# Optimization experiments

Measured on AMD Instinct MI355X. Metric: run time of the kernel, lower is better.

The kernel has to match this reference:

```python
import jax, jax.numpy as jnp
import numpy as np

K = 9          # census/SAD window (block_size arg of photometric_loss)
R = K // 2
EPS = 0.5      # loss_eps


def _grid_sample_disp(pattern, disp):
    """Disparity warp: pattern_proj[b,0,v,u] = bilinear(pattern, x=u-disp, y=v).
    Matches F.grid_sample(padding_mode='border', align_corners=True) since
    uv1 = 2*(x/(W-1)-0.5) maps back to pixel coord x exactly, and y is the row index.
    pattern: [1,1,H,W], disp: [B,H,W] -> [B,1,H,W]."""
    H, W = pattern.shape[-2:]
    B = disp.shape[0]
    u0 = jnp.arange(W, dtype=disp.dtype)
    x = u0[None, None, :] - disp                 # source x coordinate, [B,H,W]
    x = jnp.clip(x, 0.0, W - 1.0)                # border padding
    x0 = jnp.floor(x)
    w = x - x0                                   # bilinear weight
    i0 = x0.astype(jnp.int32)
    i1 = jnp.minimum(i0 + 1, W - 1)
    p = jnp.broadcast_to(pattern[0, 0], (B, H, W))
    g0 = jnp.take_along_axis(p, i0, axis=2)
    g1 = jnp.take_along_axis(p, i1, axis=2)
    return ((1.0 - w) * g0 + w * g1)[:, None]    # [B,1,H,W]


def _census_sad(a, b, eps):
    """Per-pixel census-SAD over a KxK window.
    Soft census: c(n, center) = (n-center)/(eps+|n-center|); per pixel the loss is
    mean over window offsets of |c_a - c_b|, out-of-bounds offsets skipped.
    a, b: [B,1,H,W] -> [B,1,H,W]."""
    B, C, H, W = a.shape
    pa = jnp.pad(a, ((0, 0), (0, 0), (R, R), (R, R)))
    pb = jnp.pad(b, ((0, 0), (0, 0), (R, R), (R, R)))
    vm = jnp.pad(jnp.ones((H, W), a.dtype), ((R, R), (R, R)))  # validity mask
    acc = jnp.zeros_like(a)
    for dh in range(-R, R + 1):
        for dw in range(-R, R + 1):
            na = pa[:, :, R + dh:R + dh + H, R + dw:R + dw + W]
            nb = pb[:, :, R + dh:R + dh + H, R + dw:R + dw + W]
            da = na - a
            db = nb - b
            ca = da / (eps + jnp.abs(da))
            cb = db / (eps + jnp.abs(db))
            v = vm[R + dh:R + dh + H, R + dw:R + dw + W]
            acc = acc + v * jnp.abs(ca - cb)
    return acc / (K * K)


def reference(disp0, im, pattern):
    B = disp0.shape[0]
    H, W = im.shape[-2:]
    d = disp0.reshape(B, H, W)
    pattern_proj = _grid_sample_disp(pattern, d)
    diff = _census_sad(pattern_proj, im, EPS)
    mask = jnp.ones_like(im)                     # std is None
    val = (mask * diff).sum() / mask.sum()
    return val, pattern_proj


def setup_inputs():
    key = jax.random.key(0)
    k1, k2, k3 = jax.random.split(key, 3)
    B, H, W = 32, 512, 640
    disp0 = jax.random.uniform(k1, (B, 1, H, W), dtype=jnp.float32) * 64.0
    im = jax.random.uniform(k2, (B, 1, H, W), dtype=jnp.float32)
    pattern = jax.random.uniform(k3, (1, 1, H, W), dtype=jnp.float32)
    return {"disp0": disp0, "im": im, "pattern": pattern}
```

## Files before the change

kernel.cpp:

```cpp
#include <hip/hip_runtime.h>

#define Wd 640
#define Hd 512
#define NB 32
#define TW 64
#define TH 16
#define RR 4
#define SW 72
constexpr int TILES_X = Wd / TW;
constexpr int TILES_Y = Hd / TH;
constexpr int PLANE  = (TH + RR) * SW;
constexpr float EPSC = 0.5f;

__global__ __launch_bounds__(256)
void warp_kernel(const float* __restrict__ disp, const float* __restrict__ pattern,
                 float* __restrict__ proj)
{
    int gid = blockIdx.x * 256 + threadIdx.x;
    int n = gid * 4;
    float4 d4 = *(const float4*)(disp + n);
    int u = n % Wd;
    int rowbase = ((n / Wd) % Hd) * Wd;
    float dv[4] = {d4.x, d4.y, d4.z, d4.w};
    #pragma unroll
    for (int j = 0; j < 4; ++j) {
        float x = (float)(u + j) - dv[j];
        x = fminf(fmaxf(x, 0.f), (float)(Wd - 1));
        float x0 = floorf(x);
        float w = x - x0;
        int i0 = (int)x0;
        int i1 = min(i0 + 1, Wd - 1);
        float g0 = pattern[rowbase + i0];
        float g1 = pattern[rowbase + i1];
        proj[n + j] = fmaf(w, g1 - g0, g0);
    }
}

__device__ __forceinline__ void census_ne(float na, float nb, float ac, float bc,
                                          float& n, float& e)
{
    float da = na - ac;
    float db = nb - bc;
    float d1 = EPSC + fabsf(da);
    float d2 = EPSC + fabsf(db);
    n = fmaf(da, d2, -(db * d1));
    e = d1 * d2;
}

__device__ __forceinline__ float comb4(float n1, float e1, float n2, float e2,
                                       float n3, float e3, float n4, float e4)
{
    float e12 = e1 * e2, e34 = e3 * e4;
    float s12 = fmaf(fabsf(n2), e1, fabsf(n1) * e2);
    float s34 = fmaf(fabsf(n4), e3, fabsf(n3) * e4);
    float t   = fmaf(s34, e12, s12 * e34);
    return t * __builtin_amdgcn_rcpf(e12 * e34);
}

#define WLOAD(DH) \
    a0=p0[(DH)*SW+0]; a1=p0[(DH)*SW+1]; a2=p0[(DH)*SW+2]; a3=p0[(DH)*SW+3]; \
    a4=p0[(DH)*SW+4]; a5=p0[(DH)*SW+5]; a6=p0[(DH)*SW+6]; a7=p0[(DH)*SW+7]; \
    a8=p0[(DH)*SW+8]; \
    b0=p1[(DH)*SW+0]; b1=p1[(DH)*SW+1]; b2=p1[(DH)*SW+2]; b3=p1[(DH)*SW+3]; \
    b4=p1[(DH)*SW+4]; b5=p1[(DH)*SW+5]; b6=p1[(DH)*SW+6]; b7=p1[(DH)*SW+7]; \
    b8=p1[(DH)*SW+8];

#define CENTERRT(P) { \
    cA##P = a4; cB##P = b4; \
    float n0,e0,n1,e1,n2,e2,n3,e3; \
    census_ne(a5,b5,a4,b4,n0,e0); \
    census_ne(a6,b6,a4,b4,n1,e1); \
    census_ne(a7,b7,a4,b4,n2,e2); \
    census_ne(a8,b8,a4,b4,n3,e3); \
    if constexpr (EC) { n0*=mm[5]; n1*=mm[6]; n2*=mm[7]; n3*=mm[8]; } \
    acc##P += comb4(n0,e0,n1,e1,n2,e2,n3,e3); }

#define ROWP(P) { \
    float n0,e0,n1,e1,n2,e2,n3,e3,n4,e4,n5,e5,n6,e6,n7,e7,n8,e8; \
    census_ne(a0,b0,cA##P,cB##P,n0,e0); \
    census_ne(a1,b1,cA##P,cB##P,n1,e1); \
    census_ne(a2,b2,cA##P,cB##P,n2,e2); \
    census_ne(a3,b3,cA##P,cB##P,n3,e3); \
    census_ne(a4,b4,cA##P,cB##P,n4,e4); \
    census_ne(a5,b5,cA##P,cB##P,n5,e5); \
    census_ne(a6,b6,cA##P,cB##P,n6,e6); \
    census_ne(a7,b7,cA##P,cB##P,n7,e7); \
    census_ne(a8,b8,cA##P,cB##P,n8,e8); \
    if constexpr (EC) { n0*=mm[0]; n1*=mm[1]; n2*=mm[2]; n3*=mm[3]; \
                        n5*=mm[5]; n6*=mm[6]; n7*=mm[7]; n8*=mm[8]; } \
    acc##P += comb4(n0,e0,n1,e1,n2,e2,n3,e3); \
    acc##P += comb4(n5,e5,n6,e6,n7,e7,n8,e8); \
    acc##P += fabsf(n4) * __builtin_amdgcn_rcpf(e4); }

template<bool EC>
__device__ __forceinline__ float strip_sum(const float* p0, const float* p1,
                                           int gr0, int x)
{
    float mm[9];
    if constexpr (EC) {
        #pragma unroll
        for (int i = 0; i < 9; ++i)
            mm[i] = ((unsigned)(x + i - 4) < (unsigned)Wd) ? 1.f : 0.f;
    }
    float a0,a1,a2,a3,a4,a5,a6,a7,a8, b0,b1,b2,b3,b4,b5,b6,b7,b8;
    float cA0,cA1,cA2,cA3, cB0,cB1,cB2,cB3;
    float acc0=0.f, acc1=0.f, acc2=0.f, acc3=0.f;

    WLOAD(0) CENTERRT(0)
    WLOAD(1) CENTERRT(1) ROWP(0)
    WLOAD(2) CENTERRT(2) ROWP(0) ROWP(1)
    WLOAD(3) CENTERRT(3) ROWP(0) ROWP(1) ROWP(2)
    if (gr0 + 4 < Hd) { WLOAD(4) ROWP(0) ROWP(1) ROWP(2) ROWP(3) }
    if (gr0 + 5 < Hd) { WLOAD(5) ROWP(1) ROWP(2) ROWP(3) }
    if (gr0 + 6 < Hd) { WLOAD(6) ROWP(2) ROWP(3) }
    if (gr0 + 7 < Hd) { WLOAD(7) ROWP(3) }
    return (acc0 + acc1) + (acc2 + acc3);
}

__global__ __launch_bounds__(256)
void census_kernel(const float* __restrict__ proj, const float* __restrict__ im,
                   float* __restrict__ partial)
{
    __shared__ float lds[2 * PLANE];

    const int tU = blockIdx.x, tV = blockIdx.y, b = blockIdx.z;
    const int tid = threadIdx.x;
    const float* pb = proj + (size_t)b * (Hd * Wd);
    const float* ib = im   + (size_t)b * (Hd * Wd);
    const int v0  = tV * TH;
    const int u0g = tU * TW - RR;

    const bool edgeC = (tU == 0) | (tU == TILES_X - 1);
    const bool edgeR = (tV == TILES_Y - 1);

    if (!edgeC && !edgeR) {
        const float* pbase = pb + v0 * Wd + u0g;
        const float* ibase = ib + v0 * Wd + u0g;
        for (int f = tid; f < (TH + RR) * 18; f += 256) {
            int r = f / 18;
            int c = (f - 18 * r) * 4;
            *(float4*)&lds[r * SW + c]         = *(const float4*)(pbase + r * Wd + c);
            *(float4*)&lds[PLANE + r * SW + c] = *(const float4*)(ibase + r * Wd + c);
        }
    } else {
        for (int idx = tid; idx < PLANE; idx += 256) {
            int r = idx / SW;
            int c = idx - r * SW;
            int gv = min(v0 + r, Hd - 1);
            int gu = min(max(u0g + c, 0), Wd - 1);
            int off = gv * Wd + gu;
            lds[idx]         = pb[off];
            lds[PLANE + idx] = ib[off];
        }
    }
    __syncthreads();

    const int lane = tid & 63;
    const int w    = tid >> 6;
    const int x    = tU * TW + lane;
    const int gr0  = v0 + 4 * w;
    const float* p0 = lds + (4 * w) * SW + lane;
    const float* p1 = p0 + PLANE;

    float acc = edgeC ? strip_sum<true >(p0, p1, gr0, x)
                      : strip_sum<false>(p0, p1, gr0, x);

    #pragma unroll
    for (int o = 32; o; o >>= 1) acc += __shfl_down(acc, o);
    __shared__ float wsum[4];
    if (lane == 0) wsum[w] = acc;
    __syncthreads();
    if (tid == 0) {
        float s = wsum[0] + wsum[1] + wsum[2] + wsum[3];
        partial[((int)blockIdx.z * gridDim.y + blockIdx.y) * gridDim.x + blockIdx.x] = s;
    }
}

__global__ __launch_bounds__(1024)
void final_reduce(const float* __restrict__ partial, float* __restrict__ out)
{
    const int n = NB * TILES_Y * TILES_X;
    double s = 0.0;
    for (int i = threadIdx.x; i < n; i += 1024) s += (double)partial[i];
    __shared__ double sm[1024];
    sm[threadIdx.x] = s;
    __syncthreads();
    for (int st = 512; st; st >>= 1) {
        if (threadIdx.x < st) sm[threadIdx.x] += sm[threadIdx.x + st];
        __syncthreads();
    }
    if (threadIdx.x == 0) {
        out[0] = (float)(sm[0] * (2.0 / (81.0 * (double)NB * Hd * Wd)));
    }
}

extern "C" void kernel_launch(void* const* d_in, const int* in_sizes, int n_in,
                              void* d_out, int out_size, void* d_ws, size_t ws_size,
                              hipStream_t stream)
{
    const float* disp    = (const float*)d_in[0];
    const float* im      = (const float*)d_in[1];
    const float* pattern = (const float*)d_in[2];
    float* out  = (float*)d_out;
    float* proj = out + 1;
    float* partial = (float*)d_ws;

    const int npx = NB * Hd * Wd;
    warp_kernel<<<npx / (256 * 4), 256, 0, stream>>>(disp, pattern, proj);

    dim3 grid(TILES_X, TILES_Y, NB);
    census_kernel<<<grid, 256, 0, stream>>>(proj, im, partial);

    final_reduce<<<1, 1024, 0, stream>>>(partial, out);
}
```

Baseline: 143.1 us.

## Fuse disparity warp into census kernel and switch to 4-pixel-per-thread tiling

Removes the separate warp kernel and computes the bilinear-warped pattern tile, halo included, directly into shared memory inside the census kernel. Interior pixels are also written to the proj output. This avoids writing proj and then reading it back from global memory. The tile height grows to 32 rows and each thread now handles 4 horizontal pixels with float4 LDS reads, without the previous row-reuse scheme. Halo pixels are warped redundantly across tiles, and the proj stores are scalar and misaligned (proj = out+1).

```diff
diff --git a/kernel.cpp b/kernel.cpp
--- a/kernel.cpp
+++ b/kernel.cpp
@@ -4,37 +4,14 @@
 #define Hd 512
 #define NB 32
 #define TW 64
-#define TH 16
+#define TH2 32
 #define RR 4
 #define SW 72
+#define ROWS (TH2 + RR)
 constexpr int TILES_X = Wd / TW;
-constexpr int TILES_Y = Hd / TH;
-constexpr int PLANE  = (TH + RR) * SW;
+constexpr int TILES_Y = Hd / TH2;
+constexpr int NBLK = TILES_X * TILES_Y * NB;
 constexpr float EPSC = 0.5f;
-
-__global__ __launch_bounds__(256)
-void warp_kernel(const float* __restrict__ disp, const float* __restrict__ pattern,
-                 float* __restrict__ proj)
-{
-    int gid = blockIdx.x * 256 + threadIdx.x;
-    int n = gid * 4;
-    float4 d4 = *(const float4*)(disp + n);
-    int u = n % Wd;
-    int rowbase = ((n / Wd) % Hd) * Wd;
-    float dv[4] = {d4.x, d4.y, d4.z, d4.w};
-    #pragma unroll
-    for (int j = 0; j < 4; ++j) {
-        float x = (float)(u + j) - dv[j];
-        x = fminf(fmaxf(x, 0.f), (float)(Wd - 1));
-        float x0 = floorf(x);
-        float w = x - x0;
-        int i0 = (int)x0;
-        int i1 = min(i0 + 1, Wd - 1);
-        float g0 = pattern[rowbase + i0];
-        float g1 = pattern[rowbase + i1];
-        proj[n + j] = fmaf(w, g1 - g0, g0);
-    }
-}
 
 __device__ __forceinline__ void census_ne(float na, float nb, float ac, float bc,
                                           float& n, float& e)
@@ -57,118 +34,175 @@
     return t * __builtin_amdgcn_rcpf(e12 * e34);
 }
 
-#define WLOAD(DH) \
-    a0=p0[(DH)*SW+0]; a1=p0[(DH)*SW+1]; a2=p0[(DH)*SW+2]; a3=p0[(DH)*SW+3]; \
-    a4=p0[(DH)*SW+4]; a5=p0[(DH)*SW+5]; a6=p0[(DH)*SW+6]; a7=p0[(DH)*SW+7]; \
-    a8=p0[(DH)*SW+8]; \
-    b0=p1[(DH)*SW+0]; b1=p1[(DH)*SW+1]; b2=p1[(DH)*SW+2]; b3=p1[(DH)*SW+3]; \
-    b4=p1[(DH)*SW+4]; b5=p1[(DH)*SW+5]; b6=p1[(DH)*SW+6]; b7=p1[(DH)*SW+7]; \
-    b8=p1[(DH)*SW+8];
-
-#define CENTERRT(P) { \
-    cA##P = a4; cB##P = b4; \
+#define PX_ROW(J, ACC) { \
+    float n0,e0,n1,e1,n2,e2,n3,e3,n4,e4,n5,e5,n6,e6,n7,e7,n8,e8; \
+    census_ne(wa[(J)+0],wb[(J)+0],ca[J],cb[J],n0,e0); \
+    census_ne(wa[(J)+1],wb[(J)+1],ca[J],cb[J],n1,e1); \
+    census_ne(wa[(J)+2],wb[(J)+2],ca[J],cb[J],n2,e2); \
+    census_ne(wa[(J)+3],wb[(J)+3],ca[J],cb[J],n3,e3); \
+    census_ne(wa[(J)+4],wb[(J)+4],ca[J],cb[J],n4,e4); \
+    census_ne(wa[(J)+5],wb[(J)+5],ca[J],cb[J],n5,e5); \
+    census_ne(wa[(J)+6],wb[(J)+6],ca[J],cb[J],n6,e6); \
+    census_ne(wa[(J)+7],wb[(J)+7],ca[J],cb[J],n7,e7); \
+    census_ne(wa[(J)+8],wb[(J)+8],ca[J],cb[J],n8,e8); \
+    if constexpr (EC) { n0*=m[(J)+0]; n1*=m[(J)+1]; n2*=m[(J)+2]; n3*=m[(J)+3]; \
+                        n5*=m[(J)+5]; n6*=m[(J)+6]; n7*=m[(J)+7]; n8*=m[(J)+8]; } \
+    if constexpr (ER) { n0*=mv; n1*=mv; n2*=mv; n3*=mv; n4*=mv; \
+                        n5*=mv; n6*=mv; n7*=mv; n8*=mv; } \
+    ACC += comb4(n0,e0,n1,e1,n2,e2,n3,e3); \
+    ACC += comb4(n5,e5,n6,e6,n7,e7,n8,e8); \
+    ACC = fmaf(fabsf(n4), __builtin_amdgcn_rcpf(e4), ACC); }
+
+#define PX_CTR(J, ACC) { \
     float n0,e0,n1,e1,n2,e2,n3,e3; \
-    census_ne(a5,b5,a4,b4,n0,e0); \
-    census_ne(a6,b6,a4,b4,n1,e1); \
-    census_ne(a7,b7,a4,b4,n2,e2); \
-    census_ne(a8,b8,a4,b4,n3,e3); \
-    if constexpr (EC) { n0*=mm[5]; n1*=mm[6]; n2*=mm[7]; n3*=mm[8]; } \
-    acc##P += comb4(n0,e0,n1,e1,n2,e2,n3,e3); }
-
-#define ROWP(P) { \
-    float n0,e0,n1,e1,n2,e2,n3,e3,n4,e4,n5,e5,n6,e6,n7,e7,n8,e8; \
-    census_ne(a0,b0,cA##P,cB##P,n0,e0); \
-    census_ne(a1,b1,cA##P,cB##P,n1,e1); \
-    census_ne(a2,b2,cA##P,cB##P,n2,e2); \
-    census_ne(a3,b3,cA##P,cB##P,n3,e3); \
-    census_ne(a4,b4,cA##P,cB##P,n4,e4); \
-    census_ne(a5,b5,cA##P,cB##P,n5,e5); \
-    census_ne(a6,b6,cA##P,cB##P,n6,e6); \
-    census_ne(a7,b7,cA##P,cB##P,n7,e7); \
-    census_ne(a8,b8,cA##P,cB##P,n8,e8); \
-    if constexpr (EC) { n0*=mm[0]; n1*=mm[1]; n2*=mm[2]; n3*=mm[3]; \
-                        n5*=mm[5]; n6*=mm[6]; n7*=mm[7]; n8*=mm[8]; } \
-    acc##P += comb4(n0,e0,n1,e1,n2,e2,n3,e3); \
-    acc##P += comb4(n5,e5,n6,e6,n7,e7,n8,e8); \
-    acc##P += fabsf(n4) * __builtin_amdgcn_rcpf(e4); }
-
-template<bool EC>
-__device__ __forceinline__ float strip_sum(const float* p0, const float* p1,
-                                           int gr0, int x)
-{
-    float mm[9];
+    census_ne(wa[(J)+5],wb[(J)+5],ca[J],cb[J],n0,e0); \
+    census_ne(wa[(J)+6],wb[(J)+6],ca[J],cb[J],n1,e1); \
+    census_ne(wa[(J)+7],wb[(J)+7],ca[J],cb[J],n2,e2); \
+    census_ne(wa[(J)+8],wb[(J)+8],ca[J],cb[J],n3,e3); \
+    if constexpr (EC) { n0*=m[(J)+5]; n1*=m[(J)+6]; n2*=m[(J)+7]; n3*=m[(J)+8]; } \
+    ACC += comb4(n0,e0,n1,e1,n2,e2,n3,e3); }
+
+template<bool EC, bool ER>
+__device__ __forceinline__ float strip_sum(const float (*sa)[SW], const float (*sb)[SW],
+                                           int ty, int tx, int ub, int v0)
+{
+    float m[12];
     if constexpr (EC) {
         #pragma unroll
-        for (int i = 0; i < 9; ++i)
-            mm[i] = ((unsigned)(x + i - 4) < (unsigned)Wd) ? 1.f : 0.f;
-    }
-    float a0,a1,a2,a3,a4,a5,a6,a7,a8, b0,b1,b2,b3,b4,b5,b6,b7,b8;
-    float cA0,cA1,cA2,cA3, cB0,cB1,cB2,cB3;
-    float acc0=0.f, acc1=0.f, acc2=0.f, acc3=0.f;
-
-    WLOAD(0) CENTERRT(0)
-    WLOAD(1) CENTERRT(1) ROWP(0)
-    WLOAD(2) CENTERRT(2) ROWP(0) ROWP(1)
-    WLOAD(3) CENTERRT(3) ROWP(0) ROWP(1) ROWP(2)
-    if (gr0 + 4 < Hd) { WLOAD(4) ROWP(0) ROWP(1) ROWP(2) ROWP(3) }
-    if (gr0 + 5 < Hd) { WLOAD(5) ROWP(1) ROWP(2) ROWP(3) }
-    if (gr0 + 6 < Hd) { WLOAD(6) ROWP(2) ROWP(3) }
-    if (gr0 + 7 < Hd) { WLOAD(7) ROWP(3) }
+        for (int i = 0; i < 12; ++i)
+            m[i] = ((unsigned)(ub + i - 4) < (unsigned)Wd) ? 1.f : 0.f;
+    }
+    const int cu = 4 * tx;
+    float acc0 = 0.f, acc1 = 0.f, acc2 = 0.f, acc3 = 0.f;
+
+    for (int rb = ty; rb < TH2; rb += 16) {
+        float ca[4], cb[4], wa[12], wb[12];
+        {
+            float4 A1 = *(const float4*)&sa[rb][cu + 4];
+            float4 A2 = *(const float4*)&sa[rb][cu + 8];
+            float4 B1 = *(const float4*)&sb[rb][cu + 4];
+            float4 B2 = *(const float4*)&sb[rb][cu + 8];
+            wa[4]=A1.x; wa[5]=A1.y; wa[6]=A1.z; wa[7]=A1.w;
+            wa[8]=A2.x; wa[9]=A2.y; wa[10]=A2.z; wa[11]=A2.w;
+            wb[4]=B1.x; wb[5]=B1.y; wb[6]=B1.z; wb[7]=B1.w;
+            wb[8]=B2.x; wb[9]=B2.y; wb[10]=B2.z; wb[11]=B2.w;
+            ca[0]=wa[4]; ca[1]=wa[5]; ca[2]=wa[6]; ca[3]=wa[7];
+            cb[0]=wb[4]; cb[1]=wb[5]; cb[2]=wb[6]; cb[3]=wb[7];
+            PX_CTR(0, acc0) PX_CTR(1, acc1) PX_CTR(2, acc2) PX_CTR(3, acc3)
+        }
+        for (int dh = 1; dh <= RR; ++dh) {
+            float wa[12], wb[12];
+            float4 A0 = *(const float4*)&sa[rb + dh][cu];
+            float4 A1 = *(const float4*)&sa[rb + dh][cu + 4];
+            float4 A2 = *(const float4*)&sa[rb + dh][cu + 8];
+            float4 B0 = *(const float4*)&sb[rb + dh][cu];
+            float4 B1 = *(const float4*)&sb[rb + dh][cu + 4];
+            float4 B2 = *(const float4*)&sb[rb + dh][cu + 8];
+            wa[0]=A0.x; wa[1]=A0.y; wa[2]=A0.z; wa[3]=A0.w;
+            wa[4]=A1.x; wa[5]=A1.y; wa[6]=A1.z; wa[7]=A1.w;
+            wa[8]=A2.x; wa[9]=A2.y; wa[10]=A2.z; wa[11]=A2.w;
+            wb[0]=B0.x; wb[1]=B0.y; wb[2]=B0.z; wb[3]=B0.w;
+            wb[4]=B1.x; wb[5]=B1.y; wb[6]=B1.z; wb[7]=B1.w;
+            wb[8]=B2.x; wb[9]=B2.y; wb[10]=B2.z; wb[11]=B2.w;
+            float mv = 0.f;
+            if constexpr (ER) mv = (v0 + rb + dh < Hd) ? 1.f : 0.f;
+            (void)mv;
+            PX_ROW(0, acc0) PX_ROW(1, acc1) PX_ROW(2, acc2) PX_ROW(3, acc3)
+        }
+    }
     return (acc0 + acc1) + (acc2 + acc3);
 }
 
 __global__ __launch_bounds__(256)
-void census_kernel(const float* __restrict__ proj, const float* __restrict__ im,
-                   float* __restrict__ partial)
-{
-    __shared__ float lds[2 * PLANE];
+void fused_census(const float* __restrict__ disp, const float* __restrict__ im,
+                  const float* __restrict__ pattern, float* __restrict__ proj,
+                  float* __restrict__ partial)
+{
+    __shared__ float sa[ROWS][SW];
+    __shared__ float sb[ROWS][SW];
 
     const int tU = blockIdx.x, tV = blockIdx.y, b = blockIdx.z;
     const int tid = threadIdx.x;
-    const float* pb = proj + (size_t)b * (Hd * Wd);
-    const float* ib = im   + (size_t)b * (Hd * Wd);
-    const int v0  = tV * TH;
+    const size_t HW = (size_t)Hd * Wd;
+    const float* dsp = disp + (size_t)b * HW;
+    const float* ib  = im   + (size_t)b * HW;
+    float* pj        = proj + (size_t)b * HW;
+    const int v0  = tV * TH2;
     const int u0g = tU * TW - RR;
 
     const bool edgeC = (tU == 0) | (tU == TILES_X - 1);
     const bool edgeR = (tV == TILES_Y - 1);
 
     if (!edgeC && !edgeR) {
-        const float* pbase = pb + v0 * Wd + u0g;
-        const float* ibase = ib + v0 * Wd + u0g;
-        for (int f = tid; f < (TH + RR) * 18; f += 256) {
-            int r = f / 18;
-            int c = (f - 18 * r) * 4;
-            *(float4*)&lds[r * SW + c]         = *(const float4*)(pbase + r * Wd + c);
-            *(float4*)&lds[PLANE + r * SW + c] = *(const float4*)(ibase + r * Wd + c);
+        for (int f = tid; f < ROWS * 18; f += 256) {
+            int r  = f / 18;
+            int c4 = (f - 18 * r) * 4;
+            int gy = v0 + r;
+            int gx = u0g + c4;
+            const float* prow = pattern + (size_t)gy * Wd;
+            float4 dv = *(const float4*)(dsp + (size_t)gy * Wd + gx);
+            float4 iv = *(const float4*)(ib  + (size_t)gy * Wd + gx);
+            *(float4*)&sb[r][c4] = iv;
+            float pv[4];
+            float dd[4] = {dv.x, dv.y, dv.z, dv.w};
+            #pragma unroll
+            for (int k = 0; k < 4; ++k) {
+                float x = (float)(gx + k) - dd[k];
+                x = fminf(fmaxf(x, 0.f), (float)(Wd - 1));
+                float x0 = floorf(x);
+                float w  = x - x0;
+                int i0 = (int)x0;
+                int i1 = min(i0 + 1, Wd - 1);
+                float g0 = prow[i0];
+                float g1 = prow[i1];
+                pv[k] = fmaf(w, g1 - g0, g0);
+            }
+            float4 pq = {pv[0], pv[1], pv[2], pv[3]};
+            *(float4*)&sa[r][c4] = pq;
+            if (r < TH2 && c4 >= RR && c4 <= RR + TW - 4) {
+                float* dst = pj + (size_t)gy * Wd + gx;
+                dst[0] = pv[0]; dst[1] = pv[1]; dst[2] = pv[2]; dst[3] = pv[3];
+            }
         }
     } else {
-        for (int idx = tid; idx < PLANE; idx += 256) {
+        for (int idx = tid; idx < ROWS * SW; idx += 256) {
             int r = idx / SW;
             int c = idx - r * SW;
             int gv = min(v0 + r, Hd - 1);
             int gu = min(max(u0g + c, 0), Wd - 1);
-            int off = gv * Wd + gu;
-            lds[idx]         = pb[off];
-            lds[PLANE + idx] = ib[off];
+            size_t off = (size_t)gv * Wd + gu;
+            sb[r][c] = ib[off];
+            float d = dsp[off];
+            float x = (float)gu - d;
+            x = fminf(fmaxf(x, 0.f), (float)(Wd - 1));
+            float x0 = floorf(x);
+            float w  = x - x0;
+            int i0 = (int)x0;
+            int i1 = min(i0 + 1, Wd - 1);
+            const float* prow = pattern + (size_t)gv * Wd;
+            float val = fmaf(w, prow[i1] - prow[i0], prow[i0]);
+            sa[r][c] = val;
+            if (r < TH2 && c >= RR && c < RR + TW)
+                pj[(size_t)(v0 + r) * Wd + (u0g + c)] = val;
         }
     }
     __syncthreads();
 
-    const int lane = tid & 63;
-    const int w    = tid >> 6;
-    const int x    = tU * TW + lane;
-    const int gr0  = v0 + 4 * w;
-    const float* p0 = lds + (4 * w) * SW + lane;
-    const float* p1 = p0 + PLANE;
-
-    float acc = edgeC ? strip_sum<true >(p0, p1, gr0, x)
-                      : strip_sum<false>(p0, p1, gr0, x);
+    const int ty = tid >> 4;
+    const int tx = tid & 15;
+    const int ub = tU * TW + 4 * tx;
+
+    float acc;
+    if (!edgeC && !edgeR)      acc = strip_sum<false, false>(sa, sb, ty, tx, ub, v0);
+    else if (edgeC && !edgeR)  acc = strip_sum<true,  false>(sa, sb, ty, tx, ub, v0);
+    else if (!edgeC)           acc = strip_sum<false, true >(sa, sb, ty, tx, ub, v0);
+    else                       acc = strip_sum<true,  true >(sa, sb, ty, tx, ub, v0);
 
     #pragma unroll
     for (int o = 32; o; o >>= 1) acc += __shfl_down(acc, o);
     __shared__ float wsum[4];
-    if (lane == 0) wsum[w] = acc;
+    int wid = tid >> 6, lane = tid & 63;
+    if (lane == 0) wsum[wid] = acc;
     __syncthreads();
     if (tid == 0) {
         float s = wsum[0] + wsum[1] + wsum[2] + wsum[3];
@@ -179,9 +213,8 @@
 __global__ __launch_bounds__(1024)
 void final_reduce(const float* __restrict__ partial, float* __restrict__ out)
 {
-    const int n = NB * TILES_Y * TILES_X;
     double s = 0.0;
-    for (int i = threadIdx.x; i < n; i += 1024) s += (double)partial[i];
+    for (int i = threadIdx.x; i < NBLK; i += 1024) s += (double)partial[i];
     __shared__ double sm[1024];
     sm[threadIdx.x] = s;
     __syncthreads();
@@ -205,11 +238,7 @@
     float* proj = out + 1;
     float* partial = (float*)d_ws;
 
-    const int npx = NB * Hd * Wd;
-    warp_kernel<<<npx / (256 * 4), 256, 0, stream>>>(disp, pattern, proj);
-
     dim3 grid(TILES_X, TILES_Y, NB);
-    census_kernel<<<grid, 256, 0, stream>>>(proj, im, partial);
-
+    fused_census<<<grid, 256, 0, stream>>>(disp, im, pattern, proj, partial);
     final_reduce<<<1, 1024, 0, stream>>>(partial, out);
 }
```

After: 149.0 us. 4.1% more time.
